# Optimization experiments

Hardware: AMD Instinct MI355X
Metric: run time of the kernel (lower is better)

Reference implementation:

```python
import jax, jax.numpy as jnp
import numpy as np

N, FEAT, H, D, E, C = 3072, 512, 8, 8, 100000, 2
ALPHA = 0.2  # LeakyReLU slope
NEG_INF = -9e15


def setup_inputs() -> dict:
    key = jax.random.key(0)
    ks = jax.random.split(key, 12)
    x = jax.random.normal(ks[0], (N, FEAT), dtype=jnp.float32)
    adj = (jax.random.uniform(ks[1], (N, N)) < 0.002).astype(jnp.float32)
    adj = jnp.maximum(adj, jnp.eye(N, dtype=jnp.float32))
    L = jax.random.randint(ks[2], (E,), 0, N)
    R = jax.random.randint(ks[3], (E,), 0, N)
    label = jax.random.randint(ks[4], (E,), 0, C)
    s = 1.0 / np.sqrt(FEAT)
    W = jax.random.uniform(ks[5], (H, FEAT, D), minval=-s, maxval=s, dtype=jnp.float32)
    sa = 1.0 / np.sqrt(2 * D)
    a1 = jax.random.uniform(ks[6], (H, D), minval=-sa, maxval=sa, dtype=jnp.float32)
    a2 = jax.random.uniform(ks[7], (H, D), minval=-sa, maxval=sa, dtype=jnp.float32)
    s1 = 1.0 / np.sqrt(H * D * 2)
    W1 = jax.random.uniform(ks[8], (H * D * 2, 64), minval=-s1, maxval=s1, dtype=jnp.float32)
    b1 = jnp.zeros((64,), dtype=jnp.float32)
    s2 = 1.0 / np.sqrt(64)
    W2 = jax.random.uniform(ks[9], (64, C), minval=-s2, maxval=s2, dtype=jnp.float32)
    b2 = jnp.zeros((C,), dtype=jnp.float32)
    return {"x": x, "adj": adj, "L": L, "R": R, "label": label,
            "W": W, "a1": a1, "a2": a2, "W1": W1, "b1": b1, "W2": W2, "b2": b2}


def _encoder(x, adj, W, a1, a2):
    # Wh: [H, N, D]
    Wh = jnp.einsum('nf,hfd->hnd', x, W)
    # broadcast attention logits: e[h,i,j] = leaky_relu(Wh_i.a1 + Wh_j.a2)
    s1 = jnp.einsum('hnd,hd->hn', Wh, a1)[:, :, None]   # [H,N,1]
    s2 = jnp.einsum('hnd,hd->hn', Wh, a2)[:, None, :]   # [H,1,N]
    e = jax.nn.leaky_relu(s1 + s2, negative_slope=ALPHA)  # [H,N,N]
    e = jnp.where(adj[None] > 0, e, NEG_INF)
    att = jax.nn.softmax(e, axis=-1)                      # [H,N,N]
    h = jnp.einsum('hnm,hmd->hnd', att, Wh)               # [H,N,D]
    h = jax.nn.elu(h)                                     # concat=True -> ELU
    # concat heads: [N, H*D]
    return jnp.transpose(h, (1, 0, 2)).reshape(x.shape[0], -1)


def reference(x, adj, L, R, label, W, a1, a2, W1, b1, W2, b2):
    emb = _encoder(x, adj, W, a1, a2)            # [N, 64]
    lr = jnp.concatenate([emb[L], emb[R]], axis=1)  # [E, 128]
    hcls = jax.nn.relu(lr @ W1 + b1)
    logits = hcls @ W2 + b2                       # [E, C]
    logp = jax.nn.log_softmax(logits, axis=-1)
    nll = -jnp.take_along_axis(logp, label[:, None], axis=1)[:, 0]
    return jnp.mean(nll)
```

## Files before the change

kernel.cpp:

```cpp
#include <hip/hip_runtime.h>
#include <math.h>

#define NN 3072
#define FEAT 512
#define HD 64
#define NE 100000
#define ALPHA 0.2f
#define CAP 96
#define CAPP 97
#define AROWS 8
#define WH_BLOCKS 768
#define K5_BLOCKS 2048

__global__ __launch_bounds__(256) void k_stage1(const float* __restrict__ adj, const float* __restrict__ x,
                                                const float* __restrict__ W, const float* __restrict__ a1,
                                                const float* __restrict__ a2, int* __restrict__ nbr,
                                                int* __restrict__ cnt, float* __restrict__ Wh,
                                                float* __restrict__ s1t, float* __restrict__ s2t) {
    __shared__ float xs[4][FEAT];
    __shared__ float part[4][4][HD];
    __shared__ int   wcnt[4];
    int b = blockIdx.x;
    int tid = threadIdx.x;
    int wid = tid >> 6, lane = tid & 63;

    if (b >= WH_BLOCKS) {
        int i = b - WH_BLOCKS;
        const float4* row4 = (const float4*)&adj[(size_t)i * NN];
        float4 v[3];
        #pragma unroll
        for (int c = 0; c < 3; ++c) v[c] = row4[wid * 192 + c * 64 + lane];
        unsigned long long lmask = (1ull << lane) - 1ull;
        int wc = 0;
        unsigned long long masks[12];
        #pragma unroll
        for (int c = 0; c < 3; ++c) {
            #pragma unroll
            for (int k = 0; k < 4; ++k) {
                float vk = k == 0 ? v[c].x : k == 1 ? v[c].y : k == 2 ? v[c].z : v[c].w;
                unsigned long long m = __ballot(vk > 0.f);
                masks[c * 4 + k] = m;
                wc += __popcll(m);
            }
        }
        if (lane == 0) wcnt[wid] = wc;
        __syncthreads();
        int base = 0;
        #pragma unroll
        for (int w2 = 0; w2 < 4; ++w2) if (w2 < wid) base += wcnt[w2];
        #pragma unroll
        for (int c = 0; c < 3; ++c) {
            #pragma unroll
            for (int k = 0; k < 4; ++k) {
                unsigned long long m = masks[c * 4 + k];
                if ((m >> lane) & 1ull) {
                    int pos = base + __popcll(m & lmask);
                    if (pos < CAP) nbr[i * CAP + pos] = wid * 768 + c * 256 + lane * 4 + k;
                }
                base += __popcll(m);
            }
        }
        if (tid == 0) {
            int tot = wcnt[0] + wcnt[1] + wcnt[2] + wcnt[3];
            cnt[i] = tot < CAP ? tot : CAP;
        }
    } else {
        int n0 = b * 4;
        for (int idx = tid; idx < 512; idx += 256) {
            int r = idx >> 7, fq = idx & 127;
            *(float4*)&xs[r][fq * 4] = ((const float4*)x)[(size_t)(n0 + r) * (FEAT / 4) + fq];
        }
        __syncthreads();
        int fsub = lane >> 4, h = (lane >> 1) & 7, dq = lane & 1;
        const float4* W4 = (const float4*)W;
        int base4 = h * 1024 + dq;
        int f0 = wid * (FEAT / 4);
        float4 acc0 = {0.f,0.f,0.f,0.f}, acc1 = acc0, acc2 = acc0, acc3 = acc0;
        #pragma unroll 4
        for (int f4 = 0; f4 < 32; ++f4) {
            int f = f0 + f4 * 4 + fsub;
            float4 w4 = W4[base4 + f * 2];
            float x0 = xs[0][f], x1 = xs[1][f], x2 = xs[2][f], x3 = xs[3][f];
            acc0.x = fmaf(x0, w4.x, acc0.x); acc0.y = fmaf(x0, w4.y, acc0.y);
            acc0.z = fmaf(x0, w4.z, acc0.z); acc0.w = fmaf(x0, w4.w, acc0.w);
            acc1.x = fmaf(x1, w4.x, acc1.x); acc1.y = fmaf(x1, w4.y, acc1.y);
            acc1.z = fmaf(x1, w4.z, acc1.z); acc1.w = fmaf(x1, w4.w, acc1.w);
            acc2.x = fmaf(x2, w4.x, acc2.x); acc2.y = fmaf(x2, w4.y, acc2.y);
            acc2.z = fmaf(x2, w4.z, acc2.z); acc2.w = fmaf(x2, w4.w, acc2.w);
            acc3.x = fmaf(x3, w4.x, acc3.x); acc3.y = fmaf(x3, w4.y, acc3.y);
            acc3.z = fmaf(x3, w4.z, acc3.z); acc3.w = fmaf(x3, w4.w, acc3.w);
        }
        #define RED4(A) \
            A.x += __shfl_xor(A.x, 16, 64); A.x += __shfl_xor(A.x, 32, 64); \
            A.y += __shfl_xor(A.y, 16, 64); A.y += __shfl_xor(A.y, 32, 64); \
            A.z += __shfl_xor(A.z, 16, 64); A.z += __shfl_xor(A.z, 32, 64); \
            A.w += __shfl_xor(A.w, 16, 64); A.w += __shfl_xor(A.w, 32, 64);
        RED4(acc0) RED4(acc1) RED4(acc2) RED4(acc3)
        #undef RED4
        if (fsub == 0) {
            int o = h * 8 + dq * 4;
            *(float4*)&part[wid][0][o] = acc0;
            *(float4*)&part[wid][1][o] = acc1;
            *(float4*)&part[wid][2][o] = acc2;
            *(float4*)&part[wid][3][o] = acc3;
        }
        __syncthreads();
        int n = n0 + wid;
        float v = part[0][wid][lane] + part[1][wid][lane] + part[2][wid][lane] + part[3][wid][lane];
        Wh[n * HD + lane] = v;
        float t1 = v * a1[lane];
        float t2 = v * a2[lane];
        for (int m = 1; m < 8; m <<= 1) {
            t1 += __shfl_xor(t1, m, 64);
            t2 += __shfl_xor(t2, m, 64);
        }
        if ((lane & 7) == 0) {
            int h2 = lane >> 3;
            s1t[n * 8 + h2] = t1;
            s2t[n * 8 + h2] = t2;
        }
    }
}

__global__ __launch_bounds__(512) void k_attn_pq(const float* __restrict__ Wh, const float* __restrict__ s1t,
                                                 const float* __restrict__ s2t, const int* __restrict__ nbr,
                                                 const int* __restrict__ cnt, const float* __restrict__ W1,
                                                 const float* __restrict__ b1, float* __restrict__ P,
                                                 float* __restrict__ Q) {
    __shared__ float W1s[2 * HD][HD];
    __shared__ int   jbuf[AROWS][CAP];
    __shared__ float ebuf[AROWS][8][CAPP];
    __shared__ float es[AROWS][HD];
    int tid = threadIdx.x;
    int wid = tid >> 6;
    int lane = tid & 63;
    int i = blockIdx.x * AROWS + wid;
    int h = lane >> 3, d = lane & 7;
    int ni = cnt[i];
    float s1i = s1t[i * 8 + h];
    for (int k = lane; k < CAP; k += 64)
        if (k < ni) jbuf[wid][k] = nbr[i * CAP + k];
    for (int idx = tid; idx < 2048; idx += 512)
        ((float4*)W1s)[idx] = ((const float4*)W1)[idx];
    __syncthreads();
    float mloc = -INFINITY;
    for (int k = d; k < ni; k += 8) {
        int j = jbuf[wid][k];
        float ev = s1i + s2t[j * 8 + h];
        ev = ev > 0.f ? ev : ALPHA * ev;
        ebuf[wid][h][k] = ev;
        mloc = fmaxf(mloc, ev);
    }
    mloc = fmaxf(mloc, __shfl_xor(mloc, 1, 8));
    mloc = fmaxf(mloc, __shfl_xor(mloc, 2, 8));
    mloc = fmaxf(mloc, __shfl_xor(mloc, 4, 8));
    __syncthreads();
    float denom = 0.f, acc = 0.f;
    for (int k = 0; k < ni; ++k) {
        float p = __expf(ebuf[wid][h][k] - mloc);
        denom += p;
        acc = fmaf(p, Wh[jbuf[wid][k] * HD + lane], acc);
    }
    float o = acc / denom;
    o = o > 0.f ? o : expm1f(o);
    es[wid][lane] = o;
    __syncthreads();
    float p = b1[lane], q = 0.f;
    #pragma unroll 8
    for (int k = 0; k < HD; ++k) {
        float e = es[wid][k];
        p = fmaf(e, W1s[k][lane], p);
        q = fmaf(e, W1s[HD + k][lane], q);
    }
    P[i * HD + lane] = p;
    Q[i * HD + lane] = q;
}

__global__ __launch_bounds__(256) void k_cls(const float* __restrict__ P, const float* __restrict__ Q,
                                             const int* __restrict__ L, const int* __restrict__ R,
                                             const int* __restrict__ label, const float* __restrict__ W2,
                                             const float* __restrict__ b2, float* __restrict__ partials) {
    int tid = threadIdx.x;
    int sl = tid & 15;
    int g = (blockIdx.x * 256 + tid) >> 4;
    float2 wa = *(const float2*)&W2[(sl * 4 + 0) * 2];
    float2 wb = *(const float2*)&W2[(sl * 4 + 1) * 2];
    float2 wc = *(const float2*)&W2[(sl * 4 + 2) * 2];
    float2 wd = *(const float2*)&W2[(sl * 4 + 3) * 2];
    float b20 = b2[0], b21 = b2[1];

    int e0 = g, e1 = g + 32768, e2 = g + 65536;
    int ln0 = L[e0], rn0 = R[e0], lb0 = label[e0];
    int ln1 = L[e1], rn1 = R[e1], lb1 = label[e1];
    int ln2 = L[e2], rn2 = R[e2], lb2 = label[e2];
    float4 p0 = *(const float4*)&P[ln0 * HD + sl * 4];
    float4 q0 = *(const float4*)&Q[rn0 * HD + sl * 4];
    float4 p1 = *(const float4*)&P[ln1 * HD + sl * 4];
    float4 q1 = *(const float4*)&Q[rn1 * HD + sl * 4];
    float4 p2 = *(const float4*)&P[ln2 * HD + sl * 4];
    float4 q2 = *(const float4*)&Q[rn2 * HD + sl * 4];

    float v00 = fmaxf(p0.x + q0.x, 0.f), v01 = fmaxf(p0.y + q0.y, 0.f);
    float v02 = fmaxf(p0.z + q0.z, 0.f), v03 = fmaxf(p0.w + q0.w, 0.f);
    float v10 = fmaxf(p1.x + q1.x, 0.f), v11 = fmaxf(p1.y + q1.y, 0.f);
    float v12 = fmaxf(p1.z + q1.z, 0.f), v13 = fmaxf(p1.w + q1.w, 0.f);
    float v20 = fmaxf(p2.x + q2.x, 0.f), v21 = fmaxf(p2.y + q2.y, 0.f);
    float v22 = fmaxf(p2.z + q2.z, 0.f), v23 = fmaxf(p2.w + q2.w, 0.f);

    float t00 = v00 * wa.x + v01 * wb.x + v02 * wc.x + v03 * wd.x;
    float t01 = v00 * wa.y + v01 * wb.y + v02 * wc.y + v03 * wd.y;
    float t10 = v10 * wa.x + v11 * wb.x + v12 * wc.x + v13 * wd.x;
    float t11 = v10 * wa.y + v11 * wb.y + v12 * wc.y + v13 * wd.y;
    float t20 = v20 * wa.x + v21 * wb.x + v22 * wc.x + v23 * wd.x;
    float t21 = v20 * wa.y + v21 * wb.y + v22 * wc.y + v23 * wd.y;
    #pragma unroll
    for (int m = 1; m < 16; m <<= 1) {
        t00 += __shfl_xor(t00, m, 64);  t01 += __shfl_xor(t01, m, 64);
        t10 += __shfl_xor(t10, m, 64);  t11 += __shfl_xor(t11, m, 64);
        t20 += __shfl_xor(t20, m, 64);  t21 += __shfl_xor(t21, m, 64);
    }
    float sum;
    {
        float l0 = t00 + b20, l1 = t01 + b21;
        float mx = fmaxf(l0, l1);
        sum = mx + __logf(__expf(l0 - mx) + __expf(l1 - mx)) - (lb0 ? l1 : l0);
        l0 = t10 + b20; l1 = t11 + b21; mx = fmaxf(l0, l1);
        sum += mx + __logf(__expf(l0 - mx) + __expf(l1 - mx)) - (lb1 ? l1 : l0);
        l0 = t20 + b20; l1 = t21 + b21; mx = fmaxf(l0, l1);
        sum += mx + __logf(__expf(l0 - mx) + __expf(l1 - mx)) - (lb2 ? l1 : l0);
    }
    if (g + 98304 < NE) {
        int e3 = g + 98304;
        int ln3 = L[e3], rn3 = R[e3], lb3 = label[e3];
        float4 p3 = *(const float4*)&P[ln3 * HD + sl * 4];
        float4 q3 = *(const float4*)&Q[rn3 * HD + sl * 4];
        float w0 = fmaxf(p3.x + q3.x, 0.f), w1 = fmaxf(p3.y + q3.y, 0.f);
        float w2 = fmaxf(p3.z + q3.z, 0.f), w3 = fmaxf(p3.w + q3.w, 0.f);
        float t30 = w0 * wa.x + w1 * wb.x + w2 * wc.x + w3 * wd.x;
        float t31 = w0 * wa.y + w1 * wb.y + w2 * wc.y + w3 * wd.y;
        #pragma unroll
        for (int m = 1; m < 16; m <<= 1) {
            t30 += __shfl_xor(t30, m, 64);  t31 += __shfl_xor(t31, m, 64);
        }
        float l0 = t30 + b20, l1 = t31 + b21;
        float mx = fmaxf(l0, l1);
        sum += mx + __logf(__expf(l0 - mx) + __expf(l1 - mx)) - (lb3 ? l1 : l0);
    }
    sum = (sl == 0) ? sum : 0.f;
    #pragma unroll
    for (int m = 1; m < 64; m <<= 1) sum += __shfl_xor(sum, m, 64);
    __shared__ float wsum[4];
    if ((tid & 63) == 0) wsum[tid >> 6] = sum;
    __syncthreads();
    if (tid == 0) partials[blockIdx.x] = wsum[0] + wsum[1] + wsum[2] + wsum[3];
}

__global__ __launch_bounds__(1024) void k_reduce(const float* __restrict__ partials, float* __restrict__ out) {
    __shared__ float sh[1024];
    int t = threadIdx.x;
    sh[t] = partials[t] + partials[t + 1024];
    __syncthreads();
    for (int s = 512; s > 0; s >>= 1) {
        if (t < s) sh[t] += sh[t + s];
        __syncthreads();
    }
    if (t == 0) out[0] = sh[0] / (float)NE;
}

extern "C" void kernel_launch(void* const* d_in, const int* in_sizes, int n_in,
                              void* d_out, int out_size, void* d_ws, size_t ws_size,
                              hipStream_t stream) {
    const float* x     = (const float*)d_in[0];
    const float* adj   = (const float*)d_in[1];
    const int*   L     = (const int*)d_in[2];
    const int*   R     = (const int*)d_in[3];
    const int*   label = (const int*)d_in[4];
    const float* W     = (const float*)d_in[5];
    const float* a1    = (const float*)d_in[6];
    const float* a2    = (const float*)d_in[7];
    const float* W1    = (const float*)d_in[8];
    const float* b1    = (const float*)d_in[9];
    const float* W2    = (const float*)d_in[10];
    const float* b2    = (const float*)d_in[11];

    char* ws = (char*)d_ws;
    float* Wh       = (float*)(ws + 0);
    float* s1t      = (float*)(ws + 786432);
    float* s2t      = (float*)(ws + 884736);
    int*   cnt      = (int*)  (ws + 983040);
    int*   nbr      = (int*)  (ws + 995328);
    float* P        = (float*)(ws + 2174976);
    float* Q        = (float*)(ws + 2961408);
    float* partials = (float*)(ws + 3747840);

    k_stage1<<<WH_BLOCKS + NN, 256, 0, stream>>>(adj, x, W, a1, a2, nbr, cnt, Wh, s1t, s2t);
    k_attn_pq<<<NN / AROWS, 512, 0, stream>>>(Wh, s1t, s2t, nbr, cnt, W1, b1, P, Q);
    k_cls<<<K5_BLOCKS, 256, 0, stream>>>(P, Q, L, R, label, W2, b2, partials);
    k_reduce<<<1, 1024, 0, stream>>>(partials, (float*)d_out);
}
```

Before: 34.55 us.

## Split fused stage1 into separate adjacency and Wh kernels; shrink attention blocks

Splits the fused stage1 kernel, which branched on block index between adjacency compaction and the Wh projection, into two separate kernels launched one after the other. The attention kernel now uses 4 rows per 256-thread block instead of 8 rows per 512 threads. Its neighbour aggregation loop is unrolled by two with independent accumulators to expose more memory-level parallelism. The split adds a kernel launch and serialises two stages that previously ran concurrently within one grid.

New measurement: 42.93 us. 1.24x slower.

```diff
diff --git a/kernel.cpp b/kernel.cpp
--- a/kernel.cpp
+++ b/kernel.cpp
@@ -8,121 +8,120 @@
 #define ALPHA 0.2f
 #define CAP 96
 #define CAPP 97
-#define AROWS 8
-#define WH_BLOCKS 768
+#define AROWS 4
 #define K5_BLOCKS 2048
 
-__global__ __launch_bounds__(256) void k_stage1(const float* __restrict__ adj, const float* __restrict__ x,
-                                                const float* __restrict__ W, const float* __restrict__ a1,
-                                                const float* __restrict__ a2, int* __restrict__ nbr,
-                                                int* __restrict__ cnt, float* __restrict__ Wh,
-                                                float* __restrict__ s1t, float* __restrict__ s2t) {
+__global__ __launch_bounds__(256) void k_pre(const float* __restrict__ adj, int* __restrict__ nbr,
+                                             int* __restrict__ cnt) {
+    __shared__ int wcnt[4];
+    int i = blockIdx.x;
+    int tid = threadIdx.x;
+    int wid = tid >> 6, lane = tid & 63;
+    const float4* row4 = (const float4*)&adj[(size_t)i * NN];
+    float4 v[3];
+    #pragma unroll
+    for (int c = 0; c < 3; ++c) v[c] = row4[wid * 192 + c * 64 + lane];
+    unsigned long long lmask = (1ull << lane) - 1ull;
+    int wc = 0;
+    unsigned long long masks[12];
+    #pragma unroll
+    for (int c = 0; c < 3; ++c) {
+        #pragma unroll
+        for (int k = 0; k < 4; ++k) {
+            float vk = k == 0 ? v[c].x : k == 1 ? v[c].y : k == 2 ? v[c].z : v[c].w;
+            unsigned long long m = __ballot(vk > 0.f);
+            masks[c * 4 + k] = m;
+            wc += __popcll(m);
+        }
+    }
+    if (lane == 0) wcnt[wid] = wc;
+    __syncthreads();
+    int base = 0;
+    #pragma unroll
+    for (int w2 = 0; w2 < 4; ++w2) if (w2 < wid) base += wcnt[w2];
+    #pragma unroll
+    for (int c = 0; c < 3; ++c) {
+        #pragma unroll
+        for (int k = 0; k < 4; ++k) {
+            unsigned long long m = masks[c * 4 + k];
+            if ((m >> lane) & 1ull) {
+                int pos = base + __popcll(m & lmask);
+                if (pos < CAP) nbr[i * CAP + pos] = wid * 768 + c * 256 + lane * 4 + k;
+            }
+            base += __popcll(m);
+        }
+    }
+    if (tid == 0) {
+        int tot = wcnt[0] + wcnt[1] + wcnt[2] + wcnt[3];
+        cnt[i] = tot < CAP ? tot : CAP;
+    }
+}
+
+__global__ __launch_bounds__(256) void k_wh(const float* __restrict__ x, const float* __restrict__ W,
+                                            const float* __restrict__ a1, const float* __restrict__ a2,
+                                            float* __restrict__ Wh, float* __restrict__ s1t,
+                                            float* __restrict__ s2t) {
     __shared__ float xs[4][FEAT];
     __shared__ float part[4][4][HD];
-    __shared__ int   wcnt[4];
-    int b = blockIdx.x;
     int tid = threadIdx.x;
     int wid = tid >> 6, lane = tid & 63;
-
-    if (b >= WH_BLOCKS) {
-        int i = b - WH_BLOCKS;
-        const float4* row4 = (const float4*)&adj[(size_t)i * NN];
-        float4 v[3];
-        #pragma unroll
-        for (int c = 0; c < 3; ++c) v[c] = row4[wid * 192 + c * 64 + lane];
-        unsigned long long lmask = (1ull << lane) - 1ull;
-        int wc = 0;
-        unsigned long long masks[12];
-        #pragma unroll
-        for (int c = 0; c < 3; ++c) {
-            #pragma unroll
-            for (int k = 0; k < 4; ++k) {
-                float vk = k == 0 ? v[c].x : k == 1 ? v[c].y : k == 2 ? v[c].z : v[c].w;
-                unsigned long long m = __ballot(vk > 0.f);
-                masks[c * 4 + k] = m;
-                wc += __popcll(m);
-            }
-        }
-        if (lane == 0) wcnt[wid] = wc;
-        __syncthreads();
-        int base = 0;
-        #pragma unroll
-        for (int w2 = 0; w2 < 4; ++w2) if (w2 < wid) base += wcnt[w2];
-        #pragma unroll
-        for (int c = 0; c < 3; ++c) {
-            #pragma unroll
-            for (int k = 0; k < 4; ++k) {
-                unsigned long long m = masks[c * 4 + k];
-                if ((m >> lane) & 1ull) {
-                    int pos = base + __popcll(m & lmask);
-                    if (pos < CAP) nbr[i * CAP + pos] = wid * 768 + c * 256 + lane * 4 + k;
-                }
-                base += __popcll(m);
-            }
-        }
-        if (tid == 0) {
-            int tot = wcnt[0] + wcnt[1] + wcnt[2] + wcnt[3];
-            cnt[i] = tot < CAP ? tot : CAP;
-        }
-    } else {
-        int n0 = b * 4;
-        for (int idx = tid; idx < 512; idx += 256) {
-            int r = idx >> 7, fq = idx & 127;
-            *(float4*)&xs[r][fq * 4] = ((const float4*)x)[(size_t)(n0 + r) * (FEAT / 4) + fq];
-        }
-        __syncthreads();
-        int fsub = lane >> 4, h = (lane >> 1) & 7, dq = lane & 1;
-        const float4* W4 = (const float4*)W;
-        int base4 = h * 1024 + dq;
-        int f0 = wid * (FEAT / 4);
-        float4 acc0 = {0.f,0.f,0.f,0.f}, acc1 = acc0, acc2 = acc0, acc3 = acc0;
-        #pragma unroll 4
-        for (int f4 = 0; f4 < 32; ++f4) {
-            int f = f0 + f4 * 4 + fsub;
-            float4 w4 = W4[base4 + f * 2];
-            float x0 = xs[0][f], x1 = xs[1][f], x2 = xs[2][f], x3 = xs[3][f];
-            acc0.x = fmaf(x0, w4.x, acc0.x); acc0.y = fmaf(x0, w4.y, acc0.y);
-            acc0.z = fmaf(x0, w4.z, acc0.z); acc0.w = fmaf(x0, w4.w, acc0.w);
-            acc1.x = fmaf(x1, w4.x, acc1.x); acc1.y = fmaf(x1, w4.y, acc1.y);
-            acc1.z = fmaf(x1, w4.z, acc1.z); acc1.w = fmaf(x1, w4.w, acc1.w);
-            acc2.x = fmaf(x2, w4.x, acc2.x); acc2.y = fmaf(x2, w4.y, acc2.y);
-            acc2.z = fmaf(x2, w4.z, acc2.z); acc2.w = fmaf(x2, w4.w, acc2.w);
-            acc3.x = fmaf(x3, w4.x, acc3.x); acc3.y = fmaf(x3, w4.y, acc3.y);
-            acc3.z = fmaf(x3, w4.z, acc3.z); acc3.w = fmaf(x3, w4.w, acc3.w);
-        }
-        #define RED4(A) \
-            A.x += __shfl_xor(A.x, 16, 64); A.x += __shfl_xor(A.x, 32, 64); \
-            A.y += __shfl_xor(A.y, 16, 64); A.y += __shfl_xor(A.y, 32, 64); \
-            A.z += __shfl_xor(A.z, 16, 64); A.z += __shfl_xor(A.z, 32, 64); \
-            A.w += __shfl_xor(A.w, 16, 64); A.w += __shfl_xor(A.w, 32, 64);
-        RED4(acc0) RED4(acc1) RED4(acc2) RED4(acc3)
-        #undef RED4
-        if (fsub == 0) {
-            int o = h * 8 + dq * 4;
-            *(float4*)&part[wid][0][o] = acc0;
-            *(float4*)&part[wid][1][o] = acc1;
-            *(float4*)&part[wid][2][o] = acc2;
-            *(float4*)&part[wid][3][o] = acc3;
-        }
-        __syncthreads();
-        int n = n0 + wid;
-        float v = part[0][wid][lane] + part[1][wid][lane] + part[2][wid][lane] + part[3][wid][lane];
-        Wh[n * HD + lane] = v;
-        float t1 = v * a1[lane];
-        float t2 = v * a2[lane];
-        for (int m = 1; m < 8; m <<= 1) {
-            t1 += __shfl_xor(t1, m, 64);
-            t2 += __shfl_xor(t2, m, 64);
-        }
-        if ((lane & 7) == 0) {
-            int h2 = lane >> 3;
-            s1t[n * 8 + h2] = t1;
-            s2t[n * 8 + h2] = t2;
-        }
-    }
-}
-
-__global__ __launch_bounds__(512) void k_attn_pq(const float* __restrict__ Wh, const float* __restrict__ s1t,
+    int n0 = blockIdx.x * 4;
+    for (int idx = tid; idx < 512; idx += 256) {
+        int r = idx >> 7, fq = idx & 127;
+        *(float4*)&xs[r][fq * 4] = ((const float4*)x)[(size_t)(n0 + r) * (FEAT / 4) + fq];
+    }
+    __syncthreads();
+    int fsub = lane >> 4, h = (lane >> 1) & 7, dq = lane & 1;
+    const float4* W4 = (const float4*)W;
+    int base4 = h * 1024 + dq;
+    int f0 = wid * (FEAT / 4);
+    float4 acc0 = {0.f,0.f,0.f,0.f}, acc1 = acc0, acc2 = acc0, acc3 = acc0;
+    #pragma unroll 4
+    for (int f4 = 0; f4 < 32; ++f4) {
+        int f = f0 + f4 * 4 + fsub;
+        float4 w4 = W4[base4 + f * 2];
+        float x0 = xs[0][f], x1 = xs[1][f], x2 = xs[2][f], x3 = xs[3][f];
+        acc0.x = fmaf(x0, w4.x, acc0.x); acc0.y = fmaf(x0, w4.y, acc0.y);
+        acc0.z = fmaf(x0, w4.z, acc0.z); acc0.w = fmaf(x0, w4.w, acc0.w);
+        acc1.x = fmaf(x1, w4.x, acc1.x); acc1.y = fmaf(x1, w4.y, acc1.y);
+        acc1.z = fmaf(x1, w4.z, acc1.z); acc1.w = fmaf(x1, w4.w, acc1.w);
+        acc2.x = fmaf(x2, w4.x, acc2.x); acc2.y = fmaf(x2, w4.y, acc2.y);
+        acc2.z = fmaf(x2, w4.z, acc2.z); acc2.w = fmaf(x2, w4.w, acc2.w);
+        acc3.x = fmaf(x3, w4.x, acc3.x); acc3.y = fmaf(x3, w4.y, acc3.y);
+        acc3.z = fmaf(x3, w4.z, acc3.z); acc3.w = fmaf(x3, w4.w, acc3.w);
+    }
+    #define RED4(A) \
+        A.x += __shfl_xor(A.x, 16, 64); A.x += __shfl_xor(A.x, 32, 64); \
+        A.y += __shfl_xor(A.y, 16, 64); A.y += __shfl_xor(A.y, 32, 64); \
+        A.z += __shfl_xor(A.z, 16, 64); A.z += __shfl_xor(A.z, 32, 64); \
+        A.w += __shfl_xor(A.w, 16, 64); A.w += __shfl_xor(A.w, 32, 64);
+    RED4(acc0) RED4(acc1) RED4(acc2) RED4(acc3)
+    #undef RED4
+    if (fsub == 0) {
+        int o = h * 8 + dq * 4;
+        *(float4*)&part[wid][0][o] = acc0;
+        *(float4*)&part[wid][1][o] = acc1;
+        *(float4*)&part[wid][2][o] = acc2;
+        *(float4*)&part[wid][3][o] = acc3;
+    }
+    __syncthreads();
+    int n = n0 + wid;
+    float v = part[0][wid][lane] + part[1][wid][lane] + part[2][wid][lane] + part[3][wid][lane];
+    Wh[n * HD + lane] = v;
+    float t1 = v * a1[lane];
+    float t2 = v * a2[lane];
+    for (int m = 1; m < 8; m <<= 1) {
+        t1 += __shfl_xor(t1, m, 64);
+        t2 += __shfl_xor(t2, m, 64);
+    }
+    if ((lane & 7) == 0) {
+        int h2 = lane >> 3;
+        s1t[n * 8 + h2] = t1;
+        s2t[n * 8 + h2] = t2;
+    }
+}
+
+__global__ __launch_bounds__(256) void k_attn_pq(const float* __restrict__ Wh, const float* __restrict__ s1t,
                                                  const float* __restrict__ s2t, const int* __restrict__ nbr,
                                                  const int* __restrict__ cnt, const float* __restrict__ W1,
                                                  const float* __restrict__ b1, float* __restrict__ P,
@@ -140,7 +139,7 @@
     float s1i = s1t[i * 8 + h];
     for (int k = lane; k < CAP; k += 64)
         if (k < ni) jbuf[wid][k] = nbr[i * CAP + k];
-    for (int idx = tid; idx < 2048; idx += 512)
+    for (int idx = tid; idx < 2048; idx += 256)
         ((float4*)W1s)[idx] = ((const float4*)W1)[idx];
     __syncthreads();
     float mloc = -INFINITY;
@@ -155,22 +154,32 @@
     mloc = fmaxf(mloc, __shfl_xor(mloc, 2, 8));
     mloc = fmaxf(mloc, __shfl_xor(mloc, 4, 8));
     __syncthreads();
-    float denom = 0.f, acc = 0.f;
-    for (int k = 0; k < ni; ++k) {
-        float p = __expf(ebuf[wid][h][k] - mloc);
-        denom += p;
-        acc = fmaf(p, Wh[jbuf[wid][k] * HD + lane], acc);
-    }
-    float o = acc / denom;
+    float den0 = 0.f, den1 = 0.f, ac0 = 0.f, ac1 = 0.f;
+    int k = 0;
+    for (; k + 1 < ni; k += 2) {
+        int j0 = jbuf[wid][k], j1 = jbuf[wid][k + 1];
+        float p0 = __expf(ebuf[wid][h][k] - mloc);
+        float p1 = __expf(ebuf[wid][h][k + 1] - mloc);
+        float w0 = Wh[j0 * HD + lane], w1 = Wh[j1 * HD + lane];
+        den0 += p0; den1 += p1;
+        ac0 = fmaf(p0, w0, ac0);
+        ac1 = fmaf(p1, w1, ac1);
+    }
+    if (k < ni) {
+        float p0 = __expf(ebuf[wid][h][k] - mloc);
+        den0 += p0;
+        ac0 = fmaf(p0, Wh[jbuf[wid][k] * HD + lane], ac0);
+    }
+    float o = (ac0 + ac1) / (den0 + den1);
     o = o > 0.f ? o : expm1f(o);
     es[wid][lane] = o;
     __syncthreads();
     float p = b1[lane], q = 0.f;
     #pragma unroll 8
-    for (int k = 0; k < HD; ++k) {
-        float e = es[wid][k];
-        p = fmaf(e, W1s[k][lane], p);
-        q = fmaf(e, W1s[HD + k][lane], q);
+    for (int kk = 0; kk < HD; ++kk) {
+        float e = es[wid][kk];
+        p = fmaf(e, W1s[kk][lane], p);
+        q = fmaf(e, W1s[HD + kk][lane], q);
     }
     P[i * HD + lane] = p;
     Q[i * HD + lane] = q;
@@ -293,8 +302,9 @@
     float* Q        = (float*)(ws + 2961408);
     float* partials = (float*)(ws + 3747840);
 
-    k_stage1<<<WH_BLOCKS + NN, 256, 0, stream>>>(adj, x, W, a1, a2, nbr, cnt, Wh, s1t, s2t);
-    k_attn_pq<<<NN / AROWS, 512, 0, stream>>>(Wh, s1t, s2t, nbr, cnt, W1, b1, P, Q);
+    k_pre<<<NN, 256, 0, stream>>>(adj, nbr, cnt);
+    k_wh<<<NN / 4, 256, 0, stream>>>(x, W, a1, a2, Wh, s1t, s2t);
+    k_attn_pq<<<NN / AROWS, 256, 0, stream>>>(Wh, s1t, s2t, nbr, cnt, W1, b1, P, Q);
     k_cls<<<K5_BLOCKS, 256, 0, stream>>>(P, Q, L, R, label, W2, b2, partials);
     k_reduce<<<1, 1024, 0, stream>>>(partials, (float*)d_out);
 }
```
